# Performance work log

Hardware: AMD Instinct MI355X
Metric: run time of the kernel (lower is better)

Reference implementation:

```python
import jax, jax.numpy as jnp
import numpy as np

EPS = 1e-6

def _feature_map(x):
    # elu_feature_map: elu(x) + 1
    return jax.nn.elu(x) + 1.0

def setup_inputs() -> dict:
    key = jax.random.key(0)
    ks = jax.random.split(key, 7)
    B, C, H, W = 4, 128, 32, 32
    s = 1.0 / np.sqrt(C)
    return {
        "feature": jax.random.normal(ks[0], (B, C, H, W), dtype=jnp.float32),
        "wq": jax.random.normal(ks[1], (C, C), dtype=jnp.float32) * s,
        "bq": jax.random.normal(ks[2], (C,), dtype=jnp.float32) * s,
        "wk": jax.random.normal(ks[3], (C, C), dtype=jnp.float32) * s,
        "bk": jax.random.normal(ks[4], (C,), dtype=jnp.float32) * s,
        "wv": jax.random.normal(ks[5], (C, C), dtype=jnp.float32) * s,
        "bv": jax.random.normal(ks[6], (C,), dtype=jnp.float32) * s,
    }

def reference(feature, wq, bq, wk, bk, wv, bv):
    B, C, H, W = feature.shape
    # flatten(2).transpose(1,2): (B, C, H*W) -> (B, N, C)
    x = feature.reshape(B, C, H * W).transpose(0, 2, 1)
    # torch Linear: x @ W.T + b
    query = x @ wq.T + bq
    key_p = x @ wk.T + bk
    value = x @ wv.T + bv
    Q = _feature_map(query)  # (B, N, C)
    K = _feature_map(key_p)  # (B, N, C)
    # state=None path: Si = 0 + K; Ri = 0 + outer(K, V)
    Si = K                                           # (B, N, C)
    Ri = jnp.einsum('bnc,bnm->bncm', K, value)       # (B, N, C, M)
    Z = 1.0 / (jnp.einsum('bnc,bnc->bn', Q, Si) + EPS)  # (B, N)
    RLSA = jnp.einsum('bnc,bncm,bn->bnm', Q, Ri, Z)  # (B, N, M)
    return (RLSA, Ri, Si)
```

## Files before the change

kernel.cpp:

```cpp
#include <hip/hip_runtime.h>
#include <math.h>

#define C 128
#define N 1024
#define EPS 1e-6f

#define TR 16
#define XS_STRIDE 20

__global__ __launch_bounds__(256) void qkv_kernel(
    const float* __restrict__ feat,
    const float* __restrict__ wq, const float* __restrict__ bq,
    const float* __restrict__ wk, const float* __restrict__ bk,
    const float* __restrict__ wv, const float* __restrict__ bv,
    float* __restrict__ out_rlsa, float* __restrict__ out_si,
    float* __restrict__ ws_v)
{
    __shared__ float xs[C * XS_STRIDE];
    __shared__ float sred[4][8];

    const int t    = threadIdx.x;
    const int c    = t & 127;
    const int half = t >> 7;
    const int row0 = blockIdx.x * TR;
    const int b    = row0 >> 10;
    const int n0   = row0 & 1023;

    {
        const float* fb = feat + (size_t)b * C * N;
        #pragma unroll
        for (int f = t; f < 512; f += 256) {
            int j = f >> 2, q = f & 3;
            float4 v = *(const float4*)(fb + (size_t)j * N + n0 + q * 4);
            *(float4*)&xs[j * XS_STRIDE + q * 4] = v;
        }
    }
    __syncthreads();

    float aq[8] = {0}, ak[8] = {0}, av[8] = {0};
    const float4* wq4 = (const float4*)(wq + c * C);
    const float4* wk4 = (const float4*)(wk + c * C);
    const float4* wv4 = (const float4*)(wv + c * C);
    const int xoff = half * 8;

    #pragma unroll 8
    for (int j4 = 0; j4 < 32; ++j4) {
        float4 q4 = wq4[j4];
        float4 k4 = wk4[j4];
        float4 v4 = wv4[j4];
        #pragma unroll
        for (int u = 0; u < 4; ++u) {
            const float* xr = &xs[(j4 * 4 + u) * XS_STRIDE + xoff];
            float4 xa = *(const float4*)(xr);
            float4 xb = *(const float4*)(xr + 4);
            float wqv = (u == 0) ? q4.x : (u == 1) ? q4.y : (u == 2) ? q4.z : q4.w;
            float wkv = (u == 0) ? k4.x : (u == 1) ? k4.y : (u == 2) ? k4.z : k4.w;
            float wvv = (u == 0) ? v4.x : (u == 1) ? v4.y : (u == 2) ? v4.z : v4.w;
            aq[0] += xa.x * wqv; aq[1] += xa.y * wqv; aq[2] += xa.z * wqv; aq[3] += xa.w * wqv;
            aq[4] += xb.x * wqv; aq[5] += xb.y * wqv; aq[6] += xb.z * wqv; aq[7] += xb.w * wqv;
            ak[0] += xa.x * wkv; ak[1] += xa.y * wkv; ak[2] += xa.z * wkv; ak[3] += xa.w * wkv;
            ak[4] += xb.x * wkv; ak[5] += xb.y * wkv; ak[6] += xb.z * wkv; ak[7] += xb.w * wkv;
            av[0] += xa.x * wvv; av[1] += xa.y * wvv; av[2] += xa.z * wvv; av[3] += xa.w * wvv;
            av[4] += xb.x * wvv; av[5] += xb.y * wvv; av[6] += xb.z * wvv; av[7] += xb.w * wvv;
        }
    }

    const float bqc = bq[c], bkc = bk[c], bvc = bv[c];
    float qf[8], kf[8], vf[8];
    #pragma unroll
    for (int i = 0; i < 8; ++i) {
        float q = aq[i] + bqc;
        float k = ak[i] + bkc;
        qf[i] = q > 0.f ? q + 1.f : expf(q);
        kf[i] = k > 0.f ? k + 1.f : expf(k);
        vf[i] = av[i] + bvc;
    }

    const int wave = t >> 6;
    const int lane = t & 63;
    #pragma unroll
    for (int i = 0; i < 8; ++i) {
        float p = qf[i] * kf[i];
        #pragma unroll
        for (int off = 32; off > 0; off >>= 1) p += __shfl_down(p, off, 64);
        if (lane == 0) sred[wave][i] = p;
    }
    __syncthreads();

    #pragma unroll
    for (int i = 0; i < 8; ++i) {
        float S = sred[half * 2][i] + sred[half * 2 + 1][i];
        float coef = S / (S + EPS);
        size_t ro = (size_t)(row0 + half * 8 + i) * C + c;
        out_si[ro]   = kf[i];
        out_rlsa[ro] = coef * vf[i];
        ws_v[ro]     = vf[i];
    }
}

#define BROWS 4

__global__ __launch_bounds__(256) void ri_kernel(
    const float* __restrict__ si, const float* __restrict__ ws_v,
    float* __restrict__ out_ri)
{
    __shared__ float ks[BROWS * C];
    __shared__ float vs[BROWS * C];

    const int t  = threadIdx.x;
    const int r0 = blockIdx.x * BROWS;

    #pragma unroll
    for (int idx = t; idx < BROWS * C; idx += 256) {
        int rr = idx >> 7, cc = idx & 127;
        ks[idx] = si[(size_t)(r0 + rr) * C + cc];
        vs[idx] = ws_v[(size_t)(r0 + rr) * C + cc];
    }
    __syncthreads();

    const float4* vs4 = (const float4*)vs;
    #pragma unroll
    for (int rr = 0; rr < BROWS; ++rr) {
        float4* ri4 = (float4*)(out_ri + (size_t)(r0 + rr) * C * C);
        const float* krow = ks + rr * C;
        const float4* vrow4 = vs4 + rr * 32;
        #pragma unroll
        for (int i = 0; i < 16; ++i) {
            int f4 = i * 256 + t;
            float kc = krow[f4 >> 5];
            float4 vv = vrow4[f4 & 31];
            ri4[f4] = make_float4(kc * vv.x, kc * vv.y, kc * vv.z, kc * vv.w);
        }
    }
}

extern "C" void kernel_launch(void* const* d_in, const int* in_sizes, int n_in,
                              void* d_out, int out_size, void* d_ws, size_t ws_size,
                              hipStream_t stream) {
    const float* feat = (const float*)d_in[0];
    const float* wq   = (const float*)d_in[1];
    const float* bq   = (const float*)d_in[2];
    const float* wk   = (const float*)d_in[3];
    const float* bk   = (const float*)d_in[4];
    const float* wv   = (const float*)d_in[5];
    const float* bv   = (const float*)d_in[6];

    float* out  = (float*)d_out;
    float* rlsa = out;
    float* ri   = out + (size_t)4 * 1024 * 128;
    float* si   = ri  + (size_t)4 * 1024 * 128 * 128;

    float* ws_v = (float*)d_ws;

    qkv_kernel<<<4096 / TR, 256, 0, stream>>>(feat, wq, bq, wk, bk, wv, bv,
                                              rlsa, si, ws_v);
    ri_kernel<<<4096 / BROWS, 256, 0, stream>>>(si, ws_v, ri);
}
```

Baseline: 296.4 us.

## Fuse QKV projection and Ri outer-product into one kernel with nontemporal stores

Merges the projection kernel and the Ri outer-product kernel so K and V stay in shared memory instead of going through a global workspace. Rows per block drop from 16 to 8 to give 512 blocks, and the large Ri output is written with nontemporal vector stores. This removes a kernel launch and the V/K round trip through global memory. In exchange, each block now re-reads all three weight matrices for half as many rows, and the compute and store phases are serialized within each block.

```diff
diff --git a/kernel.cpp b/kernel.cpp
--- a/kernel.cpp
+++ b/kernel.cpp
@@ -5,19 +5,23 @@
 #define N 1024
 #define EPS 1e-6f
 
-#define TR 16
-#define XS_STRIDE 20
+typedef float f32x4 __attribute__((ext_vector_type(4)));
 
-__global__ __launch_bounds__(256) void qkv_kernel(
+#define TR 8
+#define XS_STRIDE 12
+
+__global__ __launch_bounds__(256) void fused_kernel(
     const float* __restrict__ feat,
     const float* __restrict__ wq, const float* __restrict__ bq,
     const float* __restrict__ wk, const float* __restrict__ bk,
     const float* __restrict__ wv, const float* __restrict__ bv,
-    float* __restrict__ out_rlsa, float* __restrict__ out_si,
-    float* __restrict__ ws_v)
+    float* __restrict__ out_rlsa, float* __restrict__ out_ri,
+    float* __restrict__ out_si)
 {
     __shared__ float xs[C * XS_STRIDE];
-    __shared__ float sred[4][8];
+    __shared__ float sred[4][4];
+    __shared__ float ks[TR * C];
+    __shared__ float vs[TR * C];
 
     const int t    = threadIdx.x;
     const int c    = t & 127;
@@ -28,20 +32,17 @@
 
     {
         const float* fb = feat + (size_t)b * C * N;
-        #pragma unroll
-        for (int f = t; f < 512; f += 256) {
-            int j = f >> 2, q = f & 3;
-            float4 v = *(const float4*)(fb + (size_t)j * N + n0 + q * 4);
-            *(float4*)&xs[j * XS_STRIDE + q * 4] = v;
-        }
+        int j = t >> 1, q = t & 1;
+        float4 v = *(const float4*)(fb + (size_t)j * N + n0 + q * 4);
+        *(float4*)&xs[j * XS_STRIDE + q * 4] = v;
     }
     __syncthreads();
 
-    float aq[8] = {0}, ak[8] = {0}, av[8] = {0};
+    float aq[4] = {0}, ak[4] = {0}, av[4] = {0};
     const float4* wq4 = (const float4*)(wq + c * C);
     const float4* wk4 = (const float4*)(wk + c * C);
     const float4* wv4 = (const float4*)(wv + c * C);
-    const int xoff = half * 8;
+    const int xoff = half * 4;
 
     #pragma unroll 8
     for (int j4 = 0; j4 < 32; ++j4) {
@@ -50,25 +51,20 @@
         float4 v4 = wv4[j4];
         #pragma unroll
         for (int u = 0; u < 4; ++u) {
-            const float* xr = &xs[(j4 * 4 + u) * XS_STRIDE + xoff];
-            float4 xa = *(const float4*)(xr);
-            float4 xb = *(const float4*)(xr + 4);
+            float4 xa = *(const float4*)&xs[(j4 * 4 + u) * XS_STRIDE + xoff];
             float wqv = (u == 0) ? q4.x : (u == 1) ? q4.y : (u == 2) ? q4.z : q4.w;
             float wkv = (u == 0) ? k4.x : (u == 1) ? k4.y : (u == 2) ? k4.z : k4.w;
             float wvv = (u == 0) ? v4.x : (u == 1) ? v4.y : (u == 2) ? v4.z : v4.w;
             aq[0] += xa.x * wqv; aq[1] += xa.y * wqv; aq[2] += xa.z * wqv; aq[3] += xa.w * wqv;
-            aq[4] += xb.x * wqv; aq[5] += xb.y * wqv; aq[6] += xb.z * wqv; aq[7] += xb.w * wqv;
             ak[0] += xa.x * wkv; ak[1] += xa.y * wkv; ak[2] += xa.z * wkv; ak[3] += xa.w * wkv;
-            ak[4] += xb.x * wkv; ak[5] += xb.y * wkv; ak[6] += xb.z * wkv; ak[7] += xb.w * wkv;
             av[0] += xa.x * wvv; av[1] += xa.y * wvv; av[2] += xa.z * wvv; av[3] += xa.w * wvv;
-            av[4] += xb.x * wvv; av[5] += xb.y * wvv; av[6] += xb.z * wvv; av[7] += xb.w * wvv;
         }
     }
 
     const float bqc = bq[c], bkc = bk[c], bvc = bv[c];
-    float qf[8], kf[8], vf[8];
+    float qf[4], kf[4], vf[4];
     #pragma unroll
-    for (int i = 0; i < 8; ++i) {
+    for (int i = 0; i < 4; ++i) {
         float q = aq[i] + bqc;
         float k = ak[i] + bkc;
         qf[i] = q > 0.f ? q + 1.f : expf(q);
@@ -79,7 +75,7 @@
     const int wave = t >> 6;
     const int lane = t & 63;
     #pragma unroll
-    for (int i = 0; i < 8; ++i) {
+    for (int i = 0; i < 4; ++i) {
         float p = qf[i] * kf[i];
         #pragma unroll
         for (int off = 32; off > 0; off >>= 1) p += __shfl_down(p, off, 64);
@@ -88,48 +84,31 @@
     __syncthreads();
 
     #pragma unroll
-    for (int i = 0; i < 8; ++i) {
+    for (int i = 0; i < 4; ++i) {
         float S = sred[half * 2][i] + sred[half * 2 + 1][i];
         float coef = S / (S + EPS);
-        size_t ro = (size_t)(row0 + half * 8 + i) * C + c;
+        int r = half * 4 + i;
+        size_t ro = (size_t)(row0 + r) * C + c;
         out_si[ro]   = kf[i];
         out_rlsa[ro] = coef * vf[i];
-        ws_v[ro]     = vf[i];
-    }
-}
-
-#define BROWS 4
-
-__global__ __launch_bounds__(256) void ri_kernel(
-    const float* __restrict__ si, const float* __restrict__ ws_v,
-    float* __restrict__ out_ri)
-{
-    __shared__ float ks[BROWS * C];
-    __shared__ float vs[BROWS * C];
-
-    const int t  = threadIdx.x;
-    const int r0 = blockIdx.x * BROWS;
-
-    #pragma unroll
-    for (int idx = t; idx < BROWS * C; idx += 256) {
-        int rr = idx >> 7, cc = idx & 127;
-        ks[idx] = si[(size_t)(r0 + rr) * C + cc];
-        vs[idx] = ws_v[(size_t)(r0 + rr) * C + cc];
+        ks[r * C + c] = kf[i];
+        vs[r * C + c] = vf[i];
     }
     __syncthreads();
 
-    const float4* vs4 = (const float4*)vs;
+    const f32x4* vs4 = (const f32x4*)vs;
     #pragma unroll
-    for (int rr = 0; rr < BROWS; ++rr) {
-        float4* ri4 = (float4*)(out_ri + (size_t)(r0 + rr) * C * C);
-        const float* krow = ks + rr * C;
-        const float4* vrow4 = vs4 + rr * 32;
+    for (int r = 0; r < TR; ++r) {
+        f32x4* ri4 = (f32x4*)(out_ri + (size_t)(row0 + r) * C * C);
+        const float* krow  = ks  + r * C;
+        const f32x4* vrow4 = vs4 + r * 32;
         #pragma unroll
         for (int i = 0; i < 16; ++i) {
             int f4 = i * 256 + t;
             float kc = krow[f4 >> 5];
-            float4 vv = vrow4[f4 & 31];
-            ri4[f4] = make_float4(kc * vv.x, kc * vv.y, kc * vv.z, kc * vv.w);
+            f32x4 vv = vrow4[f4 & 31];
+            f32x4 o  = kc * vv;
+            __builtin_nontemporal_store(o, ri4 + f4);
         }
     }
 }
@@ -150,9 +129,6 @@
     float* ri   = out + (size_t)4 * 1024 * 128;
     float* si   = ri  + (size_t)4 * 1024 * 128 * 128;
 
-    float* ws_v = (float*)d_ws;
-
-    qkv_kernel<<<4096 / TR, 256, 0, stream>>>(feat, wq, bq, wk, bk, wv, bv,
-                                              rlsa, si, ws_v);
-    ri_kernel<<<4096 / BROWS, 256, 0, stream>>>(si, ws_v, ri);
+    fused_kernel<<<4096 / TR, 256, 0, stream>>>(feat, wq, bq, wk, bk, wv, bv,
+                                                rlsa, ri, si);
 }
```

New measurement: 308.7 us. 1.04x slower.
